# Performance work log

Measured on AMD Instinct MI355X. Metric: run time of the kernel, lower is better.

## Reference

```python
import jax, jax.numpy as jnp
import numpy as np

N_POINTS = 64
N_COLS = 500000
N_ANGS = N_POINTS * (N_POINTS - 1) // 2  # 2016


def setup_inputs() -> dict:
    key = jax.random.key(0)
    k1, k2 = jax.random.split(key)
    X = jax.random.normal(k1, (N_POINTS, N_COLS), dtype=jnp.float32)
    angles = 0.1 * jax.random.normal(k2, (N_ANGS,), dtype=jnp.float32)
    mus = jnp.ones((N_POINTS,), dtype=jnp.float32)
    return {"X": X, "angles": angles, "mus": mus}


def reference(X, angles, mus):
    # X: [n, m]; apply n(n-1)/2 sequential Givens rotations over row pairs
    # in order (iTop, iBtm) for iTop < iBtm, then scale rows by mus.
    # Original torch math per pair: vt' = c*vt - s*vb ; vb' = s*vt + c*vb.
    n = X.shape[0]
    top_np, btm_np = np.triu_indices(n, k=1)  # row-major order matches the double loop
    top = jnp.asarray(top_np, dtype=jnp.int32)
    btm = jnp.asarray(btm_np, dtype=jnp.int32)

    def step(Y, inp):
        a, it, ib = inp
        c = jnp.cos(a)
        s = jnp.sin(a)
        vt = Y[it]  # [m]
        vb = Y[ib]  # [m]
        Y = Y.at[it].set(c * vt - s * vb)
        Y = Y.at[ib].set(s * vt + c * vb)
        return Y, None

    Y, _ = jax.lax.scan(step, X, (angles, top, btm))
    return Y * mus[:, None]
```

## Files before the change

kernel.cpp:

```cpp
#include <hip/hip_runtime.h>

#define NPTS   64
#define NCOLS  500000
#define NANG   2016
#define NFULL  7812
#define TPB    512
#define BLOCKS 512
#define WSTRIDE (BLOCKS * 8)

typedef __attribute__((ext_vector_type(8))) short bf16x8;
typedef __attribute__((ext_vector_type(4))) float f32x4;

static __device__ __forceinline__ short f2bf(float f) {
    union { float f; unsigned u; } uf; uf.f = f;
    unsigned u = uf.u;
    unsigned r = (u + 0x7fffu + ((u >> 16) & 1u)) >> 16;
    return (short)r;
}

static __host__ __device__ constexpr int rotS(int i) { return 63 * i - i * (i - 1) / 2; }

__device__ __forceinline__ void chain_rolled(const float2* __restrict__ csn,
                                             float* __restrict__ P,
                                             int lane, int I0, int I1) {
    for (int r = 0; r < 64; ++r) P[r * 64 + lane] = (r == lane) ? 1.0f : 0.0f;
    int k = 0;
#pragma unroll 1
    for (int i = I0; i < I1; ++i) {
        float t = P[i * 64 + lane];
#pragma unroll 4
        for (int ib = i + 1; ib < 64; ++ib, ++k) {
            float2 cs = csn[k];
            float b = P[ib * 64 + lane];
            P[ib * 64 + lane] = cs.y * t + cs.x * b;
            t = cs.x * t - cs.y * b;
        }
        P[i * 64 + lane] = t;
    }
}

__global__ __launch_bounds__(TPB, 4) void fused_ortho(const float* __restrict__ X,
                                                      const float* __restrict__ angles,
                                                      const float* __restrict__ mus,
                                                      float* __restrict__ out) {
    __shared__ __align__(16) float sm[12288];
    const int tid  = threadIdx.x;
    const int lane = tid & 63;
    const int wave = __builtin_amdgcn_readfirstlane(tid >> 6);

    float2* csn = (float2*)sm;
    for (int t = tid; t < NANG; t += TPB) {
        float s, c;
        sincosf(angles[t], &s, &c);
        csn[t] = make_float2(c, s);
    }
    __syncthreads();

    float* P0 = sm + 4096;
    float* P1 = sm + 8192;
    if (wave == 0)      chain_rolled(csn, P0, lane, 0, 19);
    else if (wave == 1) chain_rolled(csn + rotS(19), P1, lane, 19, 63);
    __syncthreads();

    {
        const int row0 = wave * 8;
        float acc[8] = {0.f};
#pragma unroll 4
        for (int k0 = 0; k0 < 64; k0 += 4) {
            float lo0 = P0[(k0 + 0) * 64 + lane];
            float lo1 = P0[(k0 + 1) * 64 + lane];
            float lo2 = P0[(k0 + 2) * 64 + lane];
            float lo3 = P0[(k0 + 3) * 64 + lane];
#pragma unroll
            for (int r = 0; r < 8; ++r) {
                const f32x4 h = *(const f32x4*)&P1[(row0 + r) * 64 + k0];
                acc[r] = fmaf(h[0], lo0, acc[r]);
                acc[r] = fmaf(h[1], lo1, acc[r]);
                acc[r] = fmaf(h[2], lo2, acc[r]);
                acc[r] = fmaf(h[3], lo3, acc[r]);
            }
        }
#pragma unroll
        for (int r = 0; r < 8; ++r)
            sm[(row0 + r) * 64 + lane] = acc[r] * mus[row0 + r];
    }
    __syncthreads();

    const int laneN = lane & 15;
    const int quad  = lane >> 4;

    bf16x8 afrag[4][2];
#pragma unroll
    for (int t = 0; t < 4; ++t) {
#pragma unroll
        for (int q = 0; q < 2; ++q) {
            const float* src = sm + (t * 16 + laneN) * 64 + q * 32 + quad * 8;
            bf16x8 f;
#pragma unroll
            for (int j = 0; j < 8; ++j) f[j] = f2bf(src[j]);
            afrag[t][q] = f;
        }
    }

    const int gw = blockIdx.x * 8 + wave;

    for (int s = gw; s < NFULL; s += WSTRIDE) {
        const long col0 = (long)s * 64 + 4 * laneN;
        const float* xb = X + col0;

        bf16x8 bfrag[4][2];
#pragma unroll
        for (int q = 0; q < 2; ++q) {
#pragma unroll
            for (int j = 0; j < 8; ++j) {
                const int kk = q * 32 + quad * 8 + j;
                f32x4 v = *(const f32x4*)(xb + (long)kk * NCOLS);
#pragma unroll
                for (int u = 0; u < 4; ++u)
                    bfrag[u][q][j] = f2bf(v[u]);
            }
        }

#pragma unroll
        for (int t = 0; t < 4; ++t) {
            f32x4 acc[4];
#pragma unroll
            for (int u = 0; u < 4; ++u) {
                f32x4 a = {0.f, 0.f, 0.f, 0.f};
                a = __builtin_amdgcn_mfma_f32_16x16x32_bf16(afrag[t][0], bfrag[u][0], a, 0, 0, 0);
                a = __builtin_amdgcn_mfma_f32_16x16x32_bf16(afrag[t][1], bfrag[u][1], a, 0, 0, 0);
                acc[u] = a;
            }
#pragma unroll
            for (int rr = 0; rr < 4; ++rr) {
                const int row = t * 16 + quad * 4 + rr;
                f32x4 o = { acc[0][rr], acc[1][rr], acc[2][rr], acc[3][rr] };
                __builtin_nontemporal_store(o, (f32x4*)(out + (long)row * NCOLS + col0));
            }
        }
    }

    if (gw < 2) {
        const int col = NFULL * 64 + gw * 16 + laneN;
        const float* xb = X + col;
        bf16x8 bfrag[2];
#pragma unroll
        for (int q = 0; q < 2; ++q) {
            bf16x8 f;
#pragma unroll
            for (int j = 0; j < 8; ++j)
                f[j] = f2bf(xb[(long)(q * 32 + quad * 8 + j) * NCOLS]);
            bfrag[q] = f;
        }
#pragma unroll
        for (int t = 0; t < 4; ++t) {
            f32x4 a = {0.f, 0.f, 0.f, 0.f};
            a = __builtin_amdgcn_mfma_f32_16x16x32_bf16(afrag[t][0], bfrag[0], a, 0, 0, 0);
            a = __builtin_amdgcn_mfma_f32_16x16x32_bf16(afrag[t][1], bfrag[1], a, 0, 0, 0);
#pragma unroll
            for (int rr = 0; rr < 4; ++rr)
                __builtin_nontemporal_store(a[rr],
                    out + (long)(t * 16 + quad * 4 + rr) * NCOLS + col);
        }
    }
}

extern "C" void kernel_launch(void* const* d_in, const int* in_sizes, int n_in,
                              void* d_out, int out_size, void* d_ws, size_t ws_size,
                              hipStream_t stream) {
    const float* X      = (const float*)d_in[0];
    const float* angles = (const float*)d_in[1];
    const float* mus    = (const float*)d_in[2];
    fused_ortho<<<BLOCKS, TPB, 0, stream>>>(X, angles, mus, (float*)d_out);
}
```

Baseline: 269.4 us.

## Split rotation chain across three waves and use 1024-thread blocks, one tile per wave

The Givens chain is now split into three segments computed by three waves in parallel instead of two, followed by two small 64x64 matrix products to combine them. This shortens the serial prologue. Blocks grow to 1024 threads (16 waves), and the grid-stride loop is replaced by exactly one 64-column tile per wave, with tail waves handling the leftover columns. Each block still runs the serial prologue, and the larger blocks with an extra barrier-separated matmul stage may reduce occupancy or overlap.

Result: slower. 330.6 us (+22.7%).

```diff
diff --git a/kernel.cpp b/kernel.cpp
--- a/kernel.cpp
+++ b/kernel.cpp
@@ -4,9 +4,8 @@
 #define NCOLS  500000
 #define NANG   2016
 #define NFULL  7812
-#define TPB    512
+#define TPB    1024
 #define BLOCKS 512
-#define WSTRIDE (BLOCKS * 8)
 
 typedef __attribute__((ext_vector_type(8))) short bf16x8;
 typedef __attribute__((ext_vector_type(4))) float f32x4;
@@ -28,7 +27,7 @@
 #pragma unroll 1
     for (int i = I0; i < I1; ++i) {
         float t = P[i * 64 + lane];
-#pragma unroll 4
+#pragma unroll 8
         for (int ib = i + 1; ib < 64; ++ib, ++k) {
             float2 cs = csn[k];
             float b = P[ib * 64 + lane];
@@ -39,11 +38,11 @@
     }
 }
 
-__global__ __launch_bounds__(TPB, 4) void fused_ortho(const float* __restrict__ X,
+__global__ __launch_bounds__(TPB, 8) void fused_ortho(const float* __restrict__ X,
                                                       const float* __restrict__ angles,
                                                       const float* __restrict__ mus,
                                                       float* __restrict__ out) {
-    __shared__ __align__(16) float sm[12288];
+    __shared__ __align__(16) float sm[4032 + 3 * 4096];
     const int tid  = threadIdx.x;
     const int lane = tid & 63;
     const int wave = __builtin_amdgcn_readfirstlane(tid >> 6);
@@ -56,15 +55,18 @@
     }
     __syncthreads();
 
-    float* P0 = sm + 4096;
-    float* P1 = sm + 8192;
-    if (wave == 0)      chain_rolled(csn, P0, lane, 0, 19);
-    else if (wave == 1) chain_rolled(csn + rotS(19), P1, lane, 19, 63);
+    float* P0 = sm + 4032;
+    float* P1 = sm + 8128;
+    float* P2 = sm + 12224;
+
+    if (wave == 0)      chain_rolled(csn,            P0, lane,  0, 12);
+    else if (wave == 1) chain_rolled(csn + rotS(12), P1, lane, 12, 26);
+    else if (wave == 2) chain_rolled(csn + rotS(26), P2, lane, 26, 63);
     __syncthreads();
 
     {
-        const int row0 = wave * 8;
-        float acc[8] = {0.f};
+        const int row0 = wave * 4;
+        float acc[4] = {0.f, 0.f, 0.f, 0.f};
 #pragma unroll 4
         for (int k0 = 0; k0 < 64; k0 += 4) {
             float lo0 = P0[(k0 + 0) * 64 + lane];
@@ -72,7 +74,7 @@
             float lo2 = P0[(k0 + 2) * 64 + lane];
             float lo3 = P0[(k0 + 3) * 64 + lane];
 #pragma unroll
-            for (int r = 0; r < 8; ++r) {
+            for (int r = 0; r < 4; ++r) {
                 const f32x4 h = *(const f32x4*)&P1[(row0 + r) * 64 + k0];
                 acc[r] = fmaf(h[0], lo0, acc[r]);
                 acc[r] = fmaf(h[1], lo1, acc[r]);
@@ -80,9 +82,33 @@
                 acc[r] = fmaf(h[3], lo3, acc[r]);
             }
         }
-#pragma unroll
-        for (int r = 0; r < 8; ++r)
-            sm[(row0 + r) * 64 + lane] = acc[r] * mus[row0 + r];
+        __syncthreads();
+#pragma unroll
+        for (int r = 0; r < 4; ++r) P0[(row0 + r) * 64 + lane] = acc[r];
+    }
+    __syncthreads();
+
+    {
+        const int row0 = wave * 4;
+        float acc[4] = {0.f, 0.f, 0.f, 0.f};
+#pragma unroll 4
+        for (int k0 = 0; k0 < 64; k0 += 4) {
+            float lo0 = P0[(k0 + 0) * 64 + lane];
+            float lo1 = P0[(k0 + 1) * 64 + lane];
+            float lo2 = P0[(k0 + 2) * 64 + lane];
+            float lo3 = P0[(k0 + 3) * 64 + lane];
+#pragma unroll
+            for (int r = 0; r < 4; ++r) {
+                const f32x4 h = *(const f32x4*)&P2[(row0 + r) * 64 + k0];
+                acc[r] = fmaf(h[0], lo0, acc[r]);
+                acc[r] = fmaf(h[1], lo1, acc[r]);
+                acc[r] = fmaf(h[2], lo2, acc[r]);
+                acc[r] = fmaf(h[3], lo3, acc[r]);
+            }
+        }
+#pragma unroll
+        for (int r = 0; r < 4; ++r)
+            P1[(row0 + r) * 64 + lane] = acc[r] * mus[row0 + r];
     }
     __syncthreads();
 
@@ -94,7 +120,7 @@
     for (int t = 0; t < 4; ++t) {
 #pragma unroll
         for (int q = 0; q < 2; ++q) {
-            const float* src = sm + (t * 16 + laneN) * 64 + q * 32 + quad * 8;
+            const float* src = P1 + (t * 16 + laneN) * 64 + q * 32 + quad * 8;
             bf16x8 f;
 #pragma unroll
             for (int j = 0; j < 8; ++j) f[j] = f2bf(src[j]);
@@ -102,10 +128,10 @@
         }
     }
 
-    const int gw = blockIdx.x * 8 + wave;
-
-    for (int s = gw; s < NFULL; s += WSTRIDE) {
-        const long col0 = (long)s * 64 + 4 * laneN;
+    const int gw = blockIdx.x * 16 + wave;
+
+    if (gw < NFULL) {
+        const long col0 = (long)gw * 64 + 4 * laneN;
         const float* xb = X + col0;
 
         bf16x8 bfrag[4][2];
@@ -138,10 +164,9 @@
                 __builtin_nontemporal_store(o, (f32x4*)(out + (long)row * NCOLS + col0));
             }
         }
-    }
-
-    if (gw < 2) {
-        const int col = NFULL * 64 + gw * 16 + laneN;
+    } else if (gw < NFULL + 2) {
+        const int tw  = gw - NFULL;
+        const int col = NFULL * 64 + tw * 16 + laneN;
         const float* xb = X + col;
         bf16x8 bfrag[2];
 #pragma unroll
```
